# Kernel optimization log

Measured on AMD Instinct MI355X. Metric: run time of the kernel, lower is better.

Reference implementation:

```python
import jax, jax.numpy as jnp
import numpy as np

EPS = 1e-07


def setup_inputs() -> dict:
    key = jax.random.key(0)
    k1, k2, k3 = jax.random.split(key, 3)
    B, T, R, F = 16, 512, 128, 32
    timesteps = jax.random.uniform(k1, (B, T, F), dtype=jnp.float32)          # observation times, > 0
    values = jax.random.normal(k2, (B, T, F), dtype=jnp.float32)              # observed values
    reference_timesteps = jax.random.uniform(k3, (B, R), dtype=jnp.float32)  # query times
    alpha = jnp.ones((1,), dtype=jnp.float32) * 50.0                          # learned bandwidth param (init a=50)
    return {"timesteps": timesteps, "values": values,
            "reference_timesteps": reference_timesteps, "alpha": alpha}


def reference(timesteps, values, reference_timesteps, alpha):
    # timesteps, values: [B, T, F]; reference_timesteps: [B, R]; alpha: [1]
    R = reference_timesteps.shape[1]
    t = timesteps[:, None, :, :]                       # [B, 1, T, F]
    r = reference_timesteps[:, :, None, None]          # [B, R, 1, 1]
    mask = (t > 0).astype(timesteps.dtype)             # [B, 1, T, F]
    # squared-exponential kernel with mask, normalized by R (as in intensity)
    dist = jnp.exp(-alpha[0] * (r - t) ** 2) * mask + EPS  # [B, R, T, F]
    dist = dist / R
    lam = dist.sum(axis=2)                             # [B, R, F]
    smooth = jnp.sum(dist * values[:, None, :, :], axis=2) / lam  # [B, R, F]
    return smooth
```

## Files before the change

kernel.cpp:

```cpp
#include <hip/hip_runtime.h>


constexpr int B_ = 16, T_ = 512, R_ = 128, F_ = 32;
constexpr int S_  = 4;
constexpr int TS_ = T_ / S_;
constexpr int RB_ = 8;
constexpr float EPS_ = 1e-7f;

__global__ __launch_bounds__(256) void ga_partial(
    const float* __restrict__ ts_g, const float* __restrict__ v_g,
    const float* __restrict__ ref_g, const float* __restrict__ alpha_g,
    float2* __restrict__ ws)
{
    __shared__ float tile[TS_ * F_ * 2];

    const int tid = threadIdx.x;
    const int s   = blockIdx.x % S_;
    const int rb  = (blockIdx.x / S_) % (R_ / RB_);
    const int b   = blockIdx.x / (S_ * (R_ / RB_));
    const int f   = tid & 31;
    const int rl  = tid >> 5;
    const int r_idx = rb * RB_ + rl;

    const float r    = ref_g[b * R_ + r_idx];
    const float nega = -alpha_g[0];

    const float4* tsg4 = (const float4*)(ts_g + (size_t)(b * T_ + s * TS_) * F_);
    const float4* vg4  = (const float4*)(v_g  + (size_t)(b * T_ + s * TS_) * F_);
    #pragma unroll
    for (int i = tid; i < TS_ * F_ / 4; i += 256) {
        float4 a = tsg4[i];
        float4 w = vg4[i];
        a.x = (a.x > 0.f) ? a.x : 2e19f;
        a.y = (a.y > 0.f) ? a.y : 2e19f;
        a.z = (a.z > 0.f) ? a.z : 2e19f;
        a.w = (a.w > 0.f) ? a.w : 2e19f;
        float4* dst = (float4*)(tile + 8 * i);
        dst[0] = make_float4(a.x, w.x, a.y, w.y);
        dst[1] = make_float4(a.z, w.z, a.w, w.w);
    }
    __syncthreads();

    const float2* t2 = (const float2*)tile;
    float num = 0.f, den = 0.f;
    #pragma unroll 8
    for (int t = 0; t < TS_; ++t) {
        float2 tv = t2[t * F_ + f];
        float d = r - tv.x;
        float e = __expf(nega * d * d);
        float wgt = e + EPS_;
        den += wgt;
        num = fmaf(wgt, tv.y, num);
    }

    ws[(size_t)s * (B_ * R_ * F_) + (size_t)(b * R_ + r_idx) * F_ + f] =
        make_float2(num, den);
}

__global__ __launch_bounds__(256) void ga_combine(
    const float2* __restrict__ ws, float* __restrict__ out)
{
    int i = blockIdx.x * 256 + threadIdx.x;
    float num = 0.f, den = 0.f;
    #pragma unroll
    for (int s = 0; s < S_; ++s) {
        float2 p = ws[(size_t)s * (B_ * R_ * F_) + i];
        num += p.x;
        den += p.y;
    }
    out[i] = num / den;
}

extern "C" void kernel_launch(void* const* d_in, const int* in_sizes, int n_in,
                              void* d_out, int out_size, void* d_ws, size_t ws_size,
                              hipStream_t stream) {
    const float* timesteps = (const float*)d_in[0];
    const float* values    = (const float*)d_in[1];
    const float* ref_ts    = (const float*)d_in[2];
    const float* alpha     = (const float*)d_in[3];
    float* out = (float*)d_out;
    float2* ws = (float2*)d_ws;

    ga_partial<<<B_ * (R_ / RB_) * S_, 256, 0, stream>>>(
        timesteps, values, ref_ts, alpha, ws);
    ga_combine<<<(B_ * R_ * F_) / 256, 256, 0, stream>>>(ws, out);
}
```

Baseline: 69.87 us.

## Fuse partial and combine kernels into one with in-block T-split reduction

```diff
diff --git a/kernel.cpp b/kernel.cpp
--- a/kernel.cpp
+++ b/kernel.cpp
@@ -2,73 +2,74 @@
 
 
 constexpr int B_ = 16, T_ = 512, R_ = 128, F_ = 32;
-constexpr int S_  = 4;
-constexpr int TS_ = T_ / S_;
-constexpr int RB_ = 8;
+constexpr int RB_ = 4;
+constexpr int TC_ = 128;
+constexpr int NC_ = T_ / TC_;
 constexpr float EPS_ = 1e-7f;
+constexpr float LOG2E_ = 1.4426950408889634f;
 
-__global__ __launch_bounds__(256) void ga_partial(
+__global__ __launch_bounds__(256, 2) void ga_fused(
     const float* __restrict__ ts_g, const float* __restrict__ v_g,
     const float* __restrict__ ref_g, const float* __restrict__ alpha_g,
-    float2* __restrict__ ws)
+    float* __restrict__ out)
 {
-    __shared__ float tile[TS_ * F_ * 2];
+    __shared__ float2 tile[TC_ * F_];
+    __shared__ float4 red[RB_ * F_];
 
     const int tid = threadIdx.x;
-    const int s   = blockIdx.x % S_;
-    const int rb  = (blockIdx.x / S_) % (R_ / RB_);
-    const int b   = blockIdx.x / (S_ * (R_ / RB_));
     const int f   = tid & 31;
-    const int rl  = tid >> 5;
+    const int rl  = (tid >> 5) & (RB_ - 1);
+    const int th  = tid >> 7;
+    const int rb  = blockIdx.x % (R_ / RB_);
+    const int b   = blockIdx.x / (R_ / RB_);
     const int r_idx = rb * RB_ + rl;
 
-    const float r    = ref_g[b * R_ + r_idx];
-    const float nega = -alpha_g[0];
+    const float r = ref_g[b * R_ + r_idx];
+    const float c = -alpha_g[0] * LOG2E_;
 
-    const float4* tsg4 = (const float4*)(ts_g + (size_t)(b * T_ + s * TS_) * F_);
-    const float4* vg4  = (const float4*)(v_g  + (size_t)(b * T_ + s * TS_) * F_);
-    #pragma unroll
-    for (int i = tid; i < TS_ * F_ / 4; i += 256) {
-        float4 a = tsg4[i];
-        float4 w = vg4[i];
-        a.x = (a.x > 0.f) ? a.x : 2e19f;
-        a.y = (a.y > 0.f) ? a.y : 2e19f;
-        a.z = (a.z > 0.f) ? a.z : 2e19f;
-        a.w = (a.w > 0.f) ? a.w : 2e19f;
-        float4* dst = (float4*)(tile + 8 * i);
-        dst[0] = make_float4(a.x, w.x, a.y, w.y);
-        dst[1] = make_float4(a.z, w.z, a.w, w.w);
-    }
-    __syncthreads();
+    const float4* tsg4 = (const float4*)(ts_g + (size_t)b * T_ * F_);
+    const float4* vg4  = (const float4*)(v_g  + (size_t)b * T_ * F_);
 
-    const float2* t2 = (const float2*)tile;
-    float num = 0.f, den = 0.f;
-    #pragma unroll 8
-    for (int t = 0; t < TS_; ++t) {
-        float2 tv = t2[t * F_ + f];
-        float d = r - tv.x;
-        float e = __expf(nega * d * d);
-        float wgt = e + EPS_;
-        den += wgt;
-        num = fmaf(wgt, tv.y, num);
+    float num = 0.f, den = 0.f, sv = 0.f;
+
+    for (int ch = 0; ch < NC_; ++ch) {
+        if (ch) __syncthreads();
+        const int base4 = ch * (TC_ * F_ / 4);
+        #pragma unroll
+        for (int i = tid; i < TC_ * F_ / 4; i += 256) {
+            float4 a = tsg4[base4 + i];
+            float4 w = vg4[base4 + i];
+            a.x = (a.x > 0.f) ? a.x : 2e19f;
+            a.y = (a.y > 0.f) ? a.y : 2e19f;
+            a.z = (a.z > 0.f) ? a.z : 2e19f;
+            a.w = (a.w > 0.f) ? a.w : 2e19f;
+            float4* dst = (float4*)tile + 2 * i;
+            dst[0] = make_float4(a.x, w.x, a.y, w.y);
+            dst[1] = make_float4(a.z, w.z, a.w, w.w);
+        }
+        __syncthreads();
+
+        const float2* tp = tile + th * (TC_ / 2) * F_ + f;
+        #pragma unroll 16
+        for (int t = 0; t < TC_ / 2; ++t) {
+            float2 a = tp[t * F_];
+            float d = r - a.x;
+            float e = __builtin_amdgcn_exp2f(c * d * d);
+            num = fmaf(e, a.y, num);
+            den += e;
+            sv  += a.y;
+        }
     }
 
-    ws[(size_t)s * (B_ * R_ * F_) + (size_t)(b * R_ + r_idx) * F_ + f] =
-        make_float2(num, den);
-}
-
-__global__ __launch_bounds__(256) void ga_combine(
-    const float2* __restrict__ ws, float* __restrict__ out)
-{
-    int i = blockIdx.x * 256 + threadIdx.x;
-    float num = 0.f, den = 0.f;
-    #pragma unroll
-    for (int s = 0; s < S_; ++s) {
-        float2 p = ws[(size_t)s * (B_ * R_ * F_) + i];
-        num += p.x;
-        den += p.y;
+    __syncthreads();
+    if (th == 1) red[rl * F_ + f] = make_float4(num, den, sv, 0.f);
+    __syncthreads();
+    if (th == 0) {
+        float4 o = red[rl * F_ + f];
+        float n = (num + o.x) + EPS_ * (sv + o.z);
+        float d = (den + o.y) + (float)T_ * EPS_;
+        out[(b * R_ + r_idx) * F_ + f] = n / d;
     }
-    out[i] = num / den;
 }
 
 extern "C" void kernel_launch(void* const* d_in, const int* in_sizes, int n_in,
@@ -79,9 +80,7 @@
     const float* ref_ts    = (const float*)d_in[2];
     const float* alpha     = (const float*)d_in[3];
     float* out = (float*)d_out;
-    float2* ws = (float2*)d_ws;
 
-    ga_partial<<<B_ * (R_ / RB_) * S_, 256, 0, stream>>>(
-        timesteps, values, ref_ts, alpha, ws);
-    ga_combine<<<(B_ * R_ * F_) / 256, 256, 0, stream>>>(ws, out);
+    ga_fused<<<B_ * (R_ / RB_), 256, 0, stream>>>(
+        timesteps, values, ref_ts, alpha, out);
 }
```

Result: slower. 71.50 us (+2.3%).
